# Optimization experiments

Measured on AMD Instinct MI355X. Metric: run time of the kernel, lower is better.

Reference implementation:

```python
import jax, jax.numpy as jnp
import numpy as np

MAX_REL = 128  # max_relative_distance


def _rel_index(t_q, t_k, s):
    # relative_distances[i, j] = clip(i - j, -s, s) + min(s + 1, max(t_q, t_k)) - 1
    rd = jnp.arange(t_q)[:, None] - jnp.arange(t_k)[None, :]
    rd = jnp.clip(rd, -s, s)
    return rd + min(s + 1, max(t_q, t_k)) - 1  # (t_q, t_k), values in [0, 2s]


def setup_inputs() -> dict:
    key = jax.random.key(0)
    k1, k2, k3 = jax.random.split(key, 3)
    m, h, t, d = 4, 16, 1024, 128
    Q = jax.random.normal(k1, (m, h, t, d), dtype=jnp.float32)
    K = jax.random.normal(k2, (m, h, t, d), dtype=jnp.float32)
    pe = jax.random.normal(k3, (2 * MAX_REL + 1, d), dtype=jnp.float32)
    return {"Q": Q, "K": K, "pe": pe}


def reference(Q, K, pe):
    # Original: attn_rpes[t, d, s] = pe[idx[t, s], d]; out = einsum('mhtd,tds->mhts', Q, attn_rpes)
    # Equivalent (gather after matmul): out[m,h,t,s] = (Q @ pe^T)[m,h,t, idx[t,s]]
    t_q, t_k = Q.shape[2], K.shape[2]
    idx = _rel_index(t_q, t_k, MAX_REL)                     # (t_q, t_k) int32
    rel = jnp.einsum('mhtd,rd->mhtr', Q, pe)                # (m, h, t_q, 2s+1)
    out = jnp.take_along_axis(rel, idx[None, None, :, :], axis=-1)  # (m, h, t_q, t_k)
    return out
```

## Files before the change

### kernel.cpp

```cpp
#include <hip/hip_runtime.h>

constexpr int D_DIM = 128;
constexpr int T_Q   = 1024;
constexpr int NPE   = 257;
constexpr int WAVES = 8;
constexpr int BLOCK_THREADS  = WAVES * 64;
constexpr int ROWS_PER_WAVE  = 16;
constexpr int ROWS_PER_BLOCK = WAVES * ROWS_PER_WAVE;

typedef __attribute__((ext_vector_type(8))) short short8;
typedef __attribute__((ext_vector_type(4))) float f32x4;

#define RL(V, SRC) __uint_as_float(__builtin_amdgcn_readlane(__float_as_uint(V), (SRC)))

__global__ __launch_bounds__(BLOCK_THREADS, 4)
void rpe_mfma(const float* __restrict__ Q,
              const float* __restrict__ pe,
              float* __restrict__ out)
{
    __shared__ char smem_raw[NPE * 128 * 2];
    ushort* phi = reinterpret_cast<ushort*>(smem_raw);
    float (*rev)[4][264] = reinterpret_cast<float(*)[4][264]>(smem_raw);

    const int tid = threadIdx.x;
    const int w   = tid >> 6;
    const int l   = tid & 63;
    const int n15 = l & 15;
    const int g   = l >> 4;

    for (int q4 = tid; q4 < NPE * 32; q4 += BLOCK_THREADS) {
        const int n  = q4 >> 5;
        const int d0 = (q4 & 31) * 4;
        const float4 f = *reinterpret_cast<const float4*>(pe + n * 128 + d0);
        const float fv[4] = {f.x, f.y, f.z, f.w};
        ushort h[4];
#pragma unroll
        for (int e = 0; e < 4; ++e) {
            const uint u = __float_as_uint(fv[e]);
            h[e] = (ushort)((u + 0x7FFFu + ((u >> 16) & 1u)) >> 16);
        }
        const int posr0 = (d0 + 8 * (n & 15)) & 127;
        *reinterpret_cast<uint2*>(&phi[n * 128 + posr0]) = *reinterpret_cast<uint2*>(h);
    }
    __syncthreads();

    const int waveRow0 = blockIdx.x * ROWS_PER_BLOCK + w * ROWS_PER_WAVE;

    const float* qrow = Q + (size_t)(waveRow0 + n15) * D_DIM;
    short8 ahi[4], alo[4];
#pragma unroll
    for (int kk = 0; kk < 4; ++kk) {
        const int base = 32 * kk + 8 * g;
        const float4 a0 = *reinterpret_cast<const float4*>(qrow + base);
        const float4 a1 = *reinterpret_cast<const float4*>(qrow + base + 4);
        const float av[8] = {a0.x, a0.y, a0.z, a0.w, a1.x, a1.y, a1.z, a1.w};
#pragma unroll
        for (int e = 0; e < 8; ++e) {
            const uint u = __float_as_uint(av[e]);
            ahi[kk][e] = (short)(u >> 16);
            const float fl = av[e] - __uint_as_float(u & 0xffff0000u);
            alo[kk][e] = (short)(__float_as_uint(fl) >> 16);
        }
    }

    f32x4 acc[16];
#pragma unroll
    for (int j = 0; j < 16; ++j) acc[j] = (f32x4){0.f, 0.f, 0.f, 0.f};

#pragma unroll
    for (int kk = 0; kk < 4; ++kk) {
        const int posr = ((32 * kk + 8 * g) + 8 * n15) & 127;
#pragma unroll
        for (int j = 0; j < 16; ++j) {
            const short8 bh = *reinterpret_cast<const short8*>(&phi[(16 * j + n15) * 128 + posr]);
            acc[j] = __builtin_amdgcn_mfma_f32_16x16x32_bf16(ahi[kk], bh, acc[j], 0, 0, 0);
            acc[j] = __builtin_amdgcn_mfma_f32_16x16x32_bf16(alo[kk], bh, acc[j], 0, 0, 0);
        }
    }

    float rel_part = 0.f;
#pragma unroll
    for (int kk = 0; kk < 4; ++kk) {
        const short8 ph = *reinterpret_cast<const short8*>(&phi[256 * 128 + 32 * kk + 8 * g]);
#pragma unroll
        for (int e = 0; e < 8; ++e) {
            const float qv = __uint_as_float(((uint)(ushort)ahi[kk][e]) << 16)
                           + __uint_as_float(((uint)(ushort)alo[kk][e]) << 16);
            const float pv = __uint_as_float(((uint)(ushort)ph[e]) << 16);
            rel_part = fmaf(qv, pv, rel_part);
        }
    }
    rel_part += __shfl_xor(rel_part, 16, 64);
    rel_part += __shfl_xor(rel_part, 32, 64);

    __syncthreads();

#pragma unroll
    for (int c = 0; c < 4; ++c) {
#pragma unroll
        for (int j = 0; j < 16; ++j)
            rev[w][g][256 + c - 16 * j - n15] = acc[j][c];

        {
            const float rel_r = __shfl(rel_part, 4 * g + c, 64);
            const float r0_r  = __shfl(acc[0][c], 16 * g, 64);
            if (n15 <= 3) {
                if (n15 <= c) rev[w][g][n15] = rel_r;
            } else if (n15 <= 10) {
                const int p = 253 + n15;
                if (p >= 257 + c) rev[w][g][p] = r0_r;
            }
        }

#pragma unroll
        for (int u = 0; u < 4; ++u) {
            const int gRow = waveRow0 + 4 * u + c;
            const int t = gRow & (T_Q - 1);
            const int ofs = 128 - t + c;
            float* orow = out + (size_t)gRow * T_Q;
            const float rr256 = RL(rel_part, 4 * u + c);
            const float rr0   = RL(acc[0][c], 16 * u);

#pragma unroll
            for (int k = 0; k < 4; ++k) {
                const int s0 = 4 * l + 256 * k;
                const int j0 = t + 128 - s0;
                float4 v;
                if (j0 <= 0) {
                    v = make_float4(rr0, rr0, rr0, rr0);
                } else if (j0 >= 259) {
                    v = make_float4(rr256, rr256, rr256, rr256);
                } else {
                    v = *reinterpret_cast<const float4*>(&rev[w][u][s0 + ofs]);
                }
                reinterpret_cast<float4*>(orow)[l + 64 * k] = v;
            }
        }
    }
}

extern "C" void kernel_launch(void* const* d_in, const int* in_sizes, int n_in,
                              void* d_out, int out_size, void* d_ws, size_t ws_size,
                              hipStream_t stream)
{
    const float* Q  = (const float*)d_in[0];
    const float* pe = (const float*)d_in[2];
    float* out = (float*)d_out;

    const int total_rows = in_sizes[0] / D_DIM;
    const int grid = total_rows / ROWS_PER_BLOCK;
    rpe_mfma<<<grid, BLOCK_THREADS, 0, stream>>>(Q, pe, out);
}
```

Measured before the change: 77.79 us.

## Process two 16-row tiles per wave with a separate rev buffer

Result: faster. 67.60 us (-13.1%).

```diff
diff --git a/kernel.cpp b/kernel.cpp
--- a/kernel.cpp
+++ b/kernel.cpp
@@ -5,22 +5,20 @@
 constexpr int NPE   = 257;
 constexpr int WAVES = 8;
 constexpr int BLOCK_THREADS  = WAVES * 64;
-constexpr int ROWS_PER_WAVE  = 16;
-constexpr int ROWS_PER_BLOCK = WAVES * ROWS_PER_WAVE;
+constexpr int ROWS_PER_BLOCK = 256;
 
 typedef __attribute__((ext_vector_type(8))) short short8;
 typedef __attribute__((ext_vector_type(4))) float f32x4;
 
 #define RL(V, SRC) __uint_as_float(__builtin_amdgcn_readlane(__float_as_uint(V), (SRC)))
 
-__global__ __launch_bounds__(BLOCK_THREADS, 4)
+__global__ __launch_bounds__(BLOCK_THREADS, 2)
 void rpe_mfma(const float* __restrict__ Q,
               const float* __restrict__ pe,
               float* __restrict__ out)
 {
-    __shared__ char smem_raw[NPE * 128 * 2];
-    ushort* phi = reinterpret_cast<ushort*>(smem_raw);
-    float (*rev)[4][264] = reinterpret_cast<float(*)[4][264]>(smem_raw);
+    __shared__ ushort phi[NPE * 128];
+    __shared__ float  rev[WAVES][4][264];
 
     const int tid = threadIdx.x;
     const int w   = tid >> 6;
@@ -44,96 +42,102 @@
     }
     __syncthreads();
 
-    const int waveRow0 = blockIdx.x * ROWS_PER_BLOCK + w * ROWS_PER_WAVE;
+    const int waveRow0 = blockIdx.x * ROWS_PER_BLOCK + w * 32;
 
-    const float* qrow = Q + (size_t)(waveRow0 + n15) * D_DIM;
-    short8 ahi[4], alo[4];
+    short8 ahi[2][4], alo[2][4];
 #pragma unroll
-    for (int kk = 0; kk < 4; ++kk) {
-        const int base = 32 * kk + 8 * g;
-        const float4 a0 = *reinterpret_cast<const float4*>(qrow + base);
-        const float4 a1 = *reinterpret_cast<const float4*>(qrow + base + 4);
-        const float av[8] = {a0.x, a0.y, a0.z, a0.w, a1.x, a1.y, a1.z, a1.w};
+    for (int i = 0; i < 2; ++i) {
+        const float* qrow = Q + (size_t)(waveRow0 + 16 * i + n15) * D_DIM;
 #pragma unroll
-        for (int e = 0; e < 8; ++e) {
-            const uint u = __float_as_uint(av[e]);
-            ahi[kk][e] = (short)(u >> 16);
-            const float fl = av[e] - __uint_as_float(u & 0xffff0000u);
-            alo[kk][e] = (short)(__float_as_uint(fl) >> 16);
+        for (int kk = 0; kk < 4; ++kk) {
+            const int base = 32 * kk + 8 * g;
+            const float4 a0 = *reinterpret_cast<const float4*>(qrow + base);
+            const float4 a1 = *reinterpret_cast<const float4*>(qrow + base + 4);
+            const float av[8] = {a0.x, a0.y, a0.z, a0.w, a1.x, a1.y, a1.z, a1.w};
+#pragma unroll
+            for (int e = 0; e < 8; ++e) {
+                const uint u = __float_as_uint(av[e]);
+                ahi[i][kk][e] = (short)(u >> 16);
+                const float fl = av[e] - __uint_as_float(u & 0xffff0000u);
+                alo[i][kk][e] = (short)(__float_as_uint(fl) >> 16);
+            }
         }
     }
 
-    f32x4 acc[16];
 #pragma unroll
-    for (int j = 0; j < 16; ++j) acc[j] = (f32x4){0.f, 0.f, 0.f, 0.f};
+    for (int i = 0; i < 2; ++i) {
+        const int gRow0 = waveRow0 + 16 * i;
+
+        f32x4 acc[16];
+#pragma unroll
+        for (int j = 0; j < 16; ++j) acc[j] = (f32x4){0.f, 0.f, 0.f, 0.f};
 
 #pragma unroll
-    for (int kk = 0; kk < 4; ++kk) {
-        const int posr = ((32 * kk + 8 * g) + 8 * n15) & 127;
+        for (int kk = 0; kk < 4; ++kk) {
+            const int posr = ((32 * kk + 8 * g) + 8 * n15) & 127;
 #pragma unroll
-        for (int j = 0; j < 16; ++j) {
-            const short8 bh = *reinterpret_cast<const short8*>(&phi[(16 * j + n15) * 128 + posr]);
-            acc[j] = __builtin_amdgcn_mfma_f32_16x16x32_bf16(ahi[kk], bh, acc[j], 0, 0, 0);
-            acc[j] = __builtin_amdgcn_mfma_f32_16x16x32_bf16(alo[kk], bh, acc[j], 0, 0, 0);
-        }
-    }
-
-    float rel_part = 0.f;
-#pragma unroll
-    for (int kk = 0; kk < 4; ++kk) {
-        const short8 ph = *reinterpret_cast<const short8*>(&phi[256 * 128 + 32 * kk + 8 * g]);
-#pragma unroll
-        for (int e = 0; e < 8; ++e) {
-            const float qv = __uint_as_float(((uint)(ushort)ahi[kk][e]) << 16)
-                           + __uint_as_float(((uint)(ushort)alo[kk][e]) << 16);
-            const float pv = __uint_as_float(((uint)(ushort)ph[e]) << 16);
-            rel_part = fmaf(qv, pv, rel_part);
-        }
-    }
-    rel_part += __shfl_xor(rel_part, 16, 64);
-    rel_part += __shfl_xor(rel_part, 32, 64);
-
-    __syncthreads();
-
-#pragma unroll
-    for (int c = 0; c < 4; ++c) {
-#pragma unroll
-        for (int j = 0; j < 16; ++j)
-            rev[w][g][256 + c - 16 * j - n15] = acc[j][c];
-
-        {
-            const float rel_r = __shfl(rel_part, 4 * g + c, 64);
-            const float r0_r  = __shfl(acc[0][c], 16 * g, 64);
-            if (n15 <= 3) {
-                if (n15 <= c) rev[w][g][n15] = rel_r;
-            } else if (n15 <= 10) {
-                const int p = 253 + n15;
-                if (p >= 257 + c) rev[w][g][p] = r0_r;
+            for (int j = 0; j < 16; ++j) {
+                const short8 bh = *reinterpret_cast<const short8*>(&phi[(16 * j + n15) * 128 + posr]);
+                acc[j] = __builtin_amdgcn_mfma_f32_16x16x32_bf16(ahi[i][kk], bh, acc[j], 0, 0, 0);
+                acc[j] = __builtin_amdgcn_mfma_f32_16x16x32_bf16(alo[i][kk], bh, acc[j], 0, 0, 0);
             }
         }
 
+        float rel_part = 0.f;
 #pragma unroll
-        for (int u = 0; u < 4; ++u) {
-            const int gRow = waveRow0 + 4 * u + c;
-            const int t = gRow & (T_Q - 1);
-            const int ofs = 128 - t + c;
-            float* orow = out + (size_t)gRow * T_Q;
-            const float rr256 = RL(rel_part, 4 * u + c);
-            const float rr0   = RL(acc[0][c], 16 * u);
+        for (int kk = 0; kk < 4; ++kk) {
+            const short8 ph = *reinterpret_cast<const short8*>(&phi[256 * 128 + 32 * kk + 8 * g]);
+#pragma unroll
+            for (int e = 0; e < 8; ++e) {
+                const float qv = __uint_as_float(((uint)(ushort)ahi[i][kk][e]) << 16)
+                               + __uint_as_float(((uint)(ushort)alo[i][kk][e]) << 16);
+                const float pv = __uint_as_float(((uint)(ushort)ph[e]) << 16);
+                rel_part = fmaf(qv, pv, rel_part);
+            }
+        }
+        rel_part += __shfl_xor(rel_part, 16, 64);
+        rel_part += __shfl_xor(rel_part, 32, 64);
 
 #pragma unroll
-            for (int k = 0; k < 4; ++k) {
-                const int s0 = 4 * l + 256 * k;
-                const int j0 = t + 128 - s0;
-                float4 v;
-                if (j0 <= 0) {
-                    v = make_float4(rr0, rr0, rr0, rr0);
-                } else if (j0 >= 259) {
-                    v = make_float4(rr256, rr256, rr256, rr256);
-                } else {
-                    v = *reinterpret_cast<const float4*>(&rev[w][u][s0 + ofs]);
+        for (int c = 0; c < 4; ++c) {
+#pragma unroll
+            for (int j = 0; j < 16; ++j)
+                rev[w][g][256 + c - 16 * j - n15] = acc[j][c];
+
+            {
+                const float rel_r = __shfl(rel_part, 4 * g + c, 64);
+                const float r0_r  = __shfl(acc[0][c], 16 * g, 64);
+                if (n15 <= 3) {
+                    if (n15 <= c) rev[w][g][n15] = rel_r;
+                } else if (n15 <= 10) {
+                    const int p = 253 + n15;
+                    if (p >= 257 + c) rev[w][g][p] = r0_r;
                 }
-                reinterpret_cast<float4*>(orow)[l + 64 * k] = v;
+            }
+
+#pragma unroll
+            for (int u = 0; u < 4; ++u) {
+                const int gRow = gRow0 + 4 * u + c;
+                const int t = gRow & (T_Q - 1);
+                const int ofs = 128 - t + c;
+                float* orow = out + (size_t)gRow * T_Q;
+                const float rr256 = RL(rel_part, 4 * u + c);
+                const float rr0   = RL(acc[0][c], 16 * u);
+
+#pragma unroll
+                for (int k = 0; k < 4; ++k) {
+                    const int s0 = 4 * l + 256 * k;
+                    const int j0 = t + 128 - s0;
+                    float4 v;
+                    if (j0 <= 0) {
+                        v = make_float4(rr0, rr0, rr0, rr0);
+                    } else if (j0 >= 259) {
+                        v = make_float4(rr256, rr256, rr256, rr256);
+                    } else {
+                        v = *reinterpret_cast<const float4*>(&rev[w][u][s0 + ofs]);
+                    }
+                    reinterpret_cast<float4*>(orow)[l + 64 * k] = v;
+                }
             }
         }
     }
```
